# Performance work log

Measured on AMD Instinct MI355X. Metric: run time of the kernel, lower is better.

Reference implementation:

```python
import jax, jax.numpy as jnp
import numpy as np

B, S, D = 4, 2048, 512
H = 8
HD = D // H  # 64
F = 2048
EPS = 1e-12


def _layer_norm(x, g, b):
    mu = jnp.mean(x, axis=-1, keepdims=True)
    var = jnp.mean((x - mu) ** 2, axis=-1, keepdims=True)
    return (x - mu) * jax.lax.rsqrt(var + EPS) * g + b


def setup_inputs() -> dict:
    key = jax.random.key(0)
    ks = jax.random.split(key, 16)
    sd = 0.02
    inp = {
        "x": jax.random.normal(ks[0], (B, S, D), dtype=jnp.float32),
        # per-head q/k/v projections stacked: [H, D, HD] weights, [H, HD] biases
        "Wq": jax.random.normal(ks[1], (H, D, HD), dtype=jnp.float32) * sd,
        "bq": jnp.zeros((H, HD), dtype=jnp.float32),
        "Wk": jax.random.normal(ks[2], (H, D, HD), dtype=jnp.float32) * sd,
        "bk": jnp.zeros((H, HD), dtype=jnp.float32),
        "Wv": jax.random.normal(ks[3], (H, D, HD), dtype=jnp.float32) * sd,
        "bv": jnp.zeros((H, HD), dtype=jnp.float32),
        "Wo": jax.random.normal(ks[4], (D, D), dtype=jnp.float32) * sd,
        "bo": jnp.zeros((D,), dtype=jnp.float32),
        "W1": jax.random.normal(ks[5], (D, F), dtype=jnp.float32) * sd,
        "b1": jnp.zeros((F,), dtype=jnp.float32),
        "W2": jax.random.normal(ks[6], (F, D), dtype=jnp.float32) * sd,
        "b2": jnp.zeros((D,), dtype=jnp.float32),
        "ln1_g": jnp.ones((D,), dtype=jnp.float32),
        "ln1_b": jnp.zeros((D,), dtype=jnp.float32),
        "ln2_g": jnp.ones((D,), dtype=jnp.float32),
        "ln2_b": jnp.zeros((D,), dtype=jnp.float32),
    }
    return inp


def reference(x, Wq, bq, Wk, bk, Wv, bv, Wo, bo, W1, b1, W2, b2,
              ln1_g, ln1_b, ln2_g, ln2_b):
    # Multi-head attention: per-head Linear projections, batched over heads.
    q = jnp.einsum('bsd,hde->bhse', x, Wq) + bq[None, :, None, :]
    k = jnp.einsum('bsd,hde->bhse', x, Wk) + bk[None, :, None, :]
    v = jnp.einsum('bsd,hde->bhse', x, Wv) + bv[None, :, None, :]
    scores = jnp.einsum('bhse,bhte->bhst', q, k) / jnp.sqrt(jnp.float32(HD))
    weights = jax.nn.softmax(scores, axis=-1)  # [B,H,S,S] -- dominant traffic
    attn = jnp.einsum('bhst,bhte->bhse', weights, v)
    # concat heads in order along feature dim -> [B,S,D]
    concat = jnp.transpose(attn, (0, 2, 1, 3)).reshape(B, S, D)
    attn_out = concat @ Wo + bo
    # post-LN residual 1
    x1 = _layer_norm(x + attn_out, ln1_g, ln1_b)
    # FFN (exact GELU, matching torch nn.GELU default)
    h = jax.nn.gelu(x1 @ W1 + b1, approximate=False)
    ff = h @ W2 + b2
    # post-LN residual 2
    return _layer_norm(x1 + ff, ln2_g, ln2_b)
```

## Files before the change

### kernel.cpp

```cpp
#include <hip/hip_runtime.h>
#include <math.h>

#define Bb 4
#define Ss 2048
#define Dd 512
#define Hh 8
#define HDd 64
#define Ff 2048

typedef __bf16 bf16x8 __attribute__((ext_vector_type(8)));
typedef float  f32x4  __attribute__((ext_vector_type(4)));

__device__ __forceinline__ float gelu_f(float x) {
    return 0.5f * x * (1.0f + erff(x * 0.70710678118654752440f));
}

__device__ __forceinline__ unsigned short bfbits(float f) {
    __bf16 h = (__bf16)f;
    return __builtin_bit_cast(unsigned short, h);
}

__device__ __forceinline__ float b2f(unsigned short u) {
    return (float)__builtin_bit_cast(__bf16, u);
}

__device__ __forceinline__ void gld16(const unsigned short* g, unsigned short* l) {
    __builtin_amdgcn_global_load_lds(
        (const __attribute__((address_space(1))) unsigned int*)g,
        (__attribute__((address_space(3))) unsigned int*)l, 16, 0, 0);
}

__device__ __forceinline__ void tile_tconv(
    const float* __restrict__ in, unsigned short* __restrict__ out,
    int R, int C, int c0, int r0)
{
    __shared__ float tile[32][33];
    const int tx = threadIdx.x & 31, ty = threadIdx.x >> 5;
    #pragma unroll
    for (int rr = ty; rr < 32; rr += 8)
        tile[rr][tx] = in[(size_t)(r0 + rr) * C + c0 + tx];
    __syncthreads();
    #pragma unroll
    for (int cc = ty; cc < 32; cc += 8)
        out[(size_t)(c0 + cc) * R + r0 + tx] = bfbits(tile[tx][cc]);
}

__global__ __launch_bounds__(256) void prep_kernel(
    const float* __restrict__ Wq, const float* __restrict__ Wk,
    const float* __restrict__ Wv, const float* __restrict__ Wo,
    const float* __restrict__ W1, const float* __restrict__ W2,
    const float* __restrict__ x,
    unsigned short* __restrict__ WqT, unsigned short* __restrict__ WkT,
    unsigned short* __restrict__ WvT, unsigned short* __restrict__ WoT,
    unsigned short* __restrict__ W1T, unsigned short* __restrict__ W2T,
    unsigned short* __restrict__ xb)
{
    const int bid = blockIdx.x;
    if (bid < 768) {
        const float* src = bid < 256 ? Wq : (bid < 512 ? Wk : Wv);
        unsigned short* dst = bid < 256 ? WqT : (bid < 512 ? WkT : WvT);
        const int local = bid & 255;
        const int z = local >> 5;
        const int rem = local & 31;
        tile_tconv(src + (size_t)z * Dd * HDd, dst + (size_t)z * Dd * HDd,
                   Dd, HDd, (rem & 1) * 32, (rem >> 1) * 32);
    } else if (bid < 1024) {
        const int local = bid - 768;
        tile_tconv(Wo, WoT, Dd, Dd, (local & 15) * 32, (local >> 4) * 32);
    } else if (bid < 2048) {
        const int local = bid - 1024;
        tile_tconv(W1, W1T, Dd, Ff, (local & 63) * 32, (local >> 6) * 32);
    } else if (bid < 3072) {
        const int local = bid - 2048;
        tile_tconv(W2, W2T, Ff, Dd, (local & 15) * 32, (local >> 4) * 32);
    } else {
        const size_t i = ((size_t)(bid - 3072) * 256 + threadIdx.x) * 8;
        float4 a = *(const float4*)(x + i);
        float4 b = *(const float4*)(x + i + 4);
        union { unsigned short us[8]; uint4 u; } p;
        p.us[0] = bfbits(a.x); p.us[1] = bfbits(a.y);
        p.us[2] = bfbits(a.z); p.us[3] = bfbits(a.w);
        p.us[4] = bfbits(b.x); p.us[5] = bfbits(b.y);
        p.us[6] = bfbits(b.z); p.us[7] = bfbits(b.w);
        *(uint4*)(xb + i) = p.u;
    }
}

template<int ACT, int OUTBF>
__global__ __launch_bounds__(256) void gemm_mfma(
    const unsigned short* __restrict__ A, const unsigned short* __restrict__ Bt,
    const float* __restrict__ bias, void* __restrict__ C,
    int M, int N, int K)
{
    __shared__ unsigned short Asb[128 * 32];
    __shared__ unsigned short Bsb[128 * 32];
    const int t    = threadIdx.x;
    const int lane = t & 63;
    const int w    = t >> 6;
    const int ln15 = lane & 15;
    const int quad = lane >> 4;
    const int mw = (w & 1) * 64;
    const int nw = (w >> 1) * 64;
    const int m0 = blockIdx.y * 128;
    const int n0 = blockIdx.x * 128;

    const int r0c = t >> 2,           ch0 = (t & 3) << 3;
    const int r1c = (t + 256) >> 2,   ch1 = ch0;

    f32x4 acc[4][4];
    #pragma unroll
    for (int i = 0; i < 4; i++)
        #pragma unroll
        for (int j = 0; j < 4; j++) acc[i][j] = (f32x4){0.f, 0.f, 0.f, 0.f};

    for (int k0 = 0; k0 < K; k0 += 32) {
        gld16(A  + (size_t)(m0 + r0c) * K + k0 + ch0, &Asb[t * 8]);
        gld16(A  + (size_t)(m0 + r1c) * K + k0 + ch1, &Asb[(t + 256) * 8]);
        gld16(Bt + (size_t)(n0 + r0c) * K + k0 + ch0, &Bsb[t * 8]);
        gld16(Bt + (size_t)(n0 + r1c) * K + k0 + ch1, &Bsb[(t + 256) * 8]);
        __syncthreads();
        bf16x8 af[4], bf[4];
        const int kcol = quad * 8;
        #pragma unroll
        for (int i = 0; i < 4; i++)
            af[i] = *(const bf16x8*)&Asb[(mw + i * 16 + ln15) * 32 + kcol];
        #pragma unroll
        for (int j = 0; j < 4; j++)
            bf[j] = *(const bf16x8*)&Bsb[(nw + j * 16 + ln15) * 32 + kcol];
        #pragma unroll
        for (int i = 0; i < 4; i++)
            #pragma unroll
            for (int j = 0; j < 4; j++)
                acc[i][j] = __builtin_amdgcn_mfma_f32_16x16x32_bf16(
                    af[i], bf[j], acc[i][j], 0, 0, 0);
        __syncthreads();
    }

    #pragma unroll
    for (int i = 0; i < 4; i++) {
        #pragma unroll
        for (int r = 0; r < 4; r++) {
            const int m = m0 + mw + i * 16 + quad * 4 + r;
            #pragma unroll
            for (int j = 0; j < 4; j++) {
                const int n = n0 + nw + j * 16 + ln15;
                float val = acc[i][j][r] + bias[n];
                if (ACT) val = gelu_f(val);
                if (OUTBF)
                    ((unsigned short*)C)[(size_t)m * N + n] = bfbits(val);
                else
                    ((float*)C)[(size_t)m * N + n] = val;
            }
        }
    }
}

__global__ __launch_bounds__(256) void gemm_sk(
    const unsigned short* __restrict__ A, const unsigned short* __restrict__ Bt,
    const float* __restrict__ bias,
    unsigned short* __restrict__ C0, unsigned short* __restrict__ C1,
    int M, int N, int leadK, int Kslice)
{
    __shared__ unsigned short Asb[128 * 32];
    __shared__ unsigned short Bsb[128 * 32];
    const int t    = threadIdx.x;
    const int lane = t & 63;
    const int w    = t >> 6;
    const int ln15 = lane & 15;
    const int quad = lane >> 4;
    const int mw = (w & 1) * 64;
    const int nw = (w >> 1) * 64;
    const int m0 = blockIdx.y * 128;
    const int n0 = blockIdx.x * 128;
    const int z  = blockIdx.z;
    const int kbeg = z * Kslice;
    unsigned short* C = z ? C1 : C0;

    const int r0c = t >> 2,           ch0 = (t & 3) << 3;
    const int r1c = (t + 256) >> 2,   ch1 = ch0;

    f32x4 acc[4][4];
    #pragma unroll
    for (int i = 0; i < 4; i++)
        #pragma unroll
        for (int j = 0; j < 4; j++) acc[i][j] = (f32x4){0.f, 0.f, 0.f, 0.f};

    for (int k0 = kbeg; k0 < kbeg + Kslice; k0 += 32) {
        gld16(A  + (size_t)(m0 + r0c) * leadK + k0 + ch0, &Asb[t * 8]);
        gld16(A  + (size_t)(m0 + r1c) * leadK + k0 + ch1, &Asb[(t + 256) * 8]);
        gld16(Bt + (size_t)(n0 + r0c) * leadK + k0 + ch0, &Bsb[t * 8]);
        gld16(Bt + (size_t)(n0 + r1c) * leadK + k0 + ch1, &Bsb[(t + 256) * 8]);
        __syncthreads();
        bf16x8 af[4], bf[4];
        const int kcol = quad * 8;
        #pragma unroll
        for (int i = 0; i < 4; i++)
            af[i] = *(const bf16x8*)&Asb[(mw + i * 16 + ln15) * 32 + kcol];
        #pragma unroll
        for (int j = 0; j < 4; j++)
            bf[j] = *(const bf16x8*)&Bsb[(nw + j * 16 + ln15) * 32 + kcol];
        #pragma unroll
        for (int i = 0; i < 4; i++)
            #pragma unroll
            for (int j = 0; j < 4; j++)
                acc[i][j] = __builtin_amdgcn_mfma_f32_16x16x32_bf16(
                    af[i], bf[j], acc[i][j], 0, 0, 0);
        __syncthreads();
    }

    #pragma unroll
    for (int i = 0; i < 4; i++) {
        #pragma unroll
        for (int r = 0; r < 4; r++) {
            const int m = m0 + mw + i * 16 + quad * 4 + r;
            #pragma unroll
            for (int j = 0; j < 4; j++) {
                const int n = n0 + nw + j * 16 + ln15;
                const float val = acc[i][j][r] + (z == 0 ? bias[n] : 0.f);
                C[(size_t)m * N + n] = bfbits(val);
            }
        }
    }
}

__global__ __launch_bounds__(256) void qkv_mfma(
    const unsigned short* __restrict__ A,
    const unsigned short* __restrict__ WqT, const unsigned short* __restrict__ WkT,
    const unsigned short* __restrict__ WvT,
    const float* __restrict__ bq, const float* __restrict__ bk,
    const float* __restrict__ bv, unsigned short* __restrict__ qkv)
{
    const unsigned short* Bt = blockIdx.z == 0 ? WqT : (blockIdx.z == 1 ? WkT : WvT);
    const float* bias = blockIdx.z == 0 ? bq : (blockIdx.z == 1 ? bk : bv);
    unsigned short* O = qkv + (size_t)blockIdx.z * ((size_t)Bb * Hh * Ss * HDd);
    const float scl = blockIdx.z == 0 ? 0.125f * 1.44269504088896341f : 1.0f;

    __shared__ unsigned short Asb[128 * 32];
    __shared__ unsigned short Bsb[128 * 32];
    const int t    = threadIdx.x;
    const int lane = t & 63;
    const int w    = t >> 6;
    const int ln15 = lane & 15;
    const int quad = lane >> 4;
    const int mw = (w & 1) * 64;
    const int nw = (w >> 1) * 64;
    const int m0 = blockIdx.y * 128;
    const int n0 = blockIdx.x * 128;

    const int r0c = t >> 2,         ch0 = (t & 3) << 3;
    const int r1c = (t + 256) >> 2, ch1 = ch0;

    f32x4 acc[4][4];
    #pragma unroll
    for (int i = 0; i < 4; i++)
        #pragma unroll
        for (int j = 0; j < 4; j++) acc[i][j] = (f32x4){0.f, 0.f, 0.f, 0.f};

    for (int k0 = 0; k0 < Dd; k0 += 32) {
        gld16(A  + (size_t)(m0 + r0c) * Dd + k0 + ch0, &Asb[t * 8]);
        gld16(A  + (size_t)(m0 + r1c) * Dd + k0 + ch1, &Asb[(t + 256) * 8]);
        gld16(Bt + (size_t)(n0 + r0c) * Dd + k0 + ch0, &Bsb[t * 8]);
        gld16(Bt + (size_t)(n0 + r1c) * Dd + k0 + ch1, &Bsb[(t + 256) * 8]);
        __syncthreads();
        bf16x8 af[4], bf[4];
        const int kcol = quad * 8;
        #pragma unroll
        for (int i = 0; i < 4; i++)
            af[i] = *(const bf16x8*)&Asb[(mw + i * 16 + ln15) * 32 + kcol];
        #pragma unroll
        for (int j = 0; j < 4; j++)
            bf[j] = *(const bf16x8*)&Bsb[(nw + j * 16 + ln15) * 32 + kcol];
        #pragma unroll
        for (int i = 0; i < 4; i++)
            #pragma unroll
            for (int j = 0; j < 4; j++)
                acc[i][j] = __builtin_amdgcn_mfma_f32_16x16x32_bf16(
                    af[i], bf[j], acc[i][j], 0, 0, 0);
        __syncthreads();
    }

    if (blockIdx.z == 2) {
        #pragma unroll
        for (int i = 0; i < 4; i++) {
            const int mb = m0 + mw + i * 16 + quad * 4;
            const int bI = mb >> 11;
            const int sI = mb & 2047;
            #pragma unroll
            for (int j = 0; j < 4; j++) {
                const int n = n0 + nw + j * 16 + ln15;
                union { unsigned short us[4]; uint2 u2; } pk;
                #pragma unroll
                for (int r = 0; r < 4; r++)
                    pk.us[r] = bfbits(acc[i][j][r] + bias[n]);
                *(uint2*)&O[(((size_t)bI * Hh + (n >> 6)) * HDd + (n & 63)) * Ss + sI]
                    = pk.u2;
            }
        }
    } else {
        #pragma unroll
        for (int i = 0; i < 4; i++) {
            #pragma unroll
            for (int r = 0; r < 4; r++) {
                const int m  = m0 + mw + i * 16 + quad * 4 + r;
                const int bI = m >> 11;
                const int sI = m & 2047;
                #pragma unroll
                for (int j = 0; j < 4; j++) {
                    const int n = n0 + nw + j * 16 + ln15;
                    const float val = (acc[i][j][r] + bias[n]) * scl;
                    O[(((size_t)bI * Hh + (n >> 6)) * Ss + sI) * HDd + (n & 63)] =
                        bfbits(val);
                }
            }
        }
    }
}

__global__ __launch_bounds__(256) void attn_mfma(
    const unsigned short* __restrict__ q, const unsigned short* __restrict__ k,
    const unsigned short* __restrict__ vt, unsigned short* __restrict__ out)
{
    __shared__ unsigned short Ks[64 * 64];
    __shared__ unsigned short VTs[64 * 64];
    __shared__ unsigned short Ps[64][72];
    __shared__ float lrow[4][16];
    const int t    = threadIdx.x;
    const int lane = t & 63;
    const int w    = t >> 6;
    const int ln15 = lane & 15;
    const int quad = lane >> 4;
    const int qw   = w * 16;
    const int h = blockIdx.y, b = blockIdx.z;
    const int q0 = blockIdx.x * 64;
    const unsigned short* qb  = q  + (((size_t)b * Hh + h) * Ss + q0) * HDd;
    const unsigned short* kb  = k  + ((size_t)b * Hh + h) * Ss * HDd;
    const unsigned short* vtb = vt + ((size_t)b * Hh + h) * HDd * Ss;

    const int sr0 = t >> 3,         sch0 = (t & 7) << 3;
    const int sr1 = (t + 256) >> 3, sch1 = sch0;

    const bf16x8 qf0 = *(const bf16x8*)(qb + (size_t)(qw + ln15) * HDd + quad * 8);
    const bf16x8 qf1 = *(const bf16x8*)(qb + (size_t)(qw + ln15) * HDd + 32 + quad * 8);

    f32x4 o_acc[4];
    #pragma unroll
    for (int s = 0; s < 4; s++) o_acc[s] = (f32x4){0.f, 0.f, 0.f, 0.f};
    float l_run = 0.f;

    for (int kt = 0; kt < Ss; kt += 64) {
        __syncthreads();
        gld16(kb  + (size_t)(kt + sr0) * HDd + sch0, &Ks[t * 8]);
        gld16(kb  + (size_t)(kt + sr1) * HDd + sch1, &Ks[(t + 256) * 8]);
        gld16(vtb + (size_t)sr0 * Ss + kt + sch0, &VTs[t * 8]);
        gld16(vtb + (size_t)sr1 * Ss + kt + sch1, &VTs[(t + 256) * 8]);
        __syncthreads();

        f32x4 sc[4];
        #pragma unroll
        for (int s = 0; s < 4; s++) {
            const bf16x8 ka  = *(const bf16x8*)&Ks[(s * 16 + ln15) * 64 + quad * 8];
            const bf16x8 kb2 = *(const bf16x8*)&Ks[(s * 16 + ln15) * 64 + 32 + quad * 8];
            f32x4 z = (f32x4){0.f, 0.f, 0.f, 0.f};
            z = __builtin_amdgcn_mfma_f32_16x16x32_bf16(ka, qf0, z, 0, 0, 0);
            sc[s] = __builtin_amdgcn_mfma_f32_16x16x32_bf16(kb2, qf1, z, 0, 0, 0);
        }

        #pragma unroll
        for (int s = 0; s < 4; s++)
            #pragma unroll
            for (int r = 0; r < 4; r++) {
                sc[s][r] = exp2f(sc[s][r]);
                l_run += sc[s][r];
            }

        #pragma unroll
        for (int s = 0; s < 4; s++) {
            union { unsigned short us[4]; uint2 u2; } pk;
            #pragma unroll
            for (int r = 0; r < 4; r++) pk.us[r] = bfbits(sc[s][r]);
            *(uint2*)&Ps[qw + ln15][s * 16 + quad * 4] = pk.u2;
        }

        const bf16x8 pf0 = *(const bf16x8*)&Ps[qw + ln15][quad * 8];
        const bf16x8 pf1 = *(const bf16x8*)&Ps[qw + ln15][32 + quad * 8];
        #pragma unroll
        for (int s = 0; s < 4; s++) {
            const bf16x8 v0 = *(const bf16x8*)&VTs[(s * 16 + ln15) * 64 + quad * 8];
            const bf16x8 v1 = *(const bf16x8*)&VTs[(s * 16 + ln15) * 64 + 32 + quad * 8];
            o_acc[s] = __builtin_amdgcn_mfma_f32_16x16x32_bf16(pf0, v0, o_acc[s], 0, 0, 0);
            o_acc[s] = __builtin_amdgcn_mfma_f32_16x16x32_bf16(pf1, v1, o_acc[s], 0, 0, 0);
        }
    }

    l_run += __shfl_xor(l_run, 16);
    l_run += __shfl_xor(l_run, 32);
    if (quad == 0) lrow[w][ln15] = l_run;
    const float4 lv = *(const float4*)&lrow[w][quad * 4];
    const float inv[4] = {1.f / lv.x, 1.f / lv.y, 1.f / lv.z, 1.f / lv.w};
    #pragma unroll
    for (int r = 0; r < 4; r++) {
        const int row = q0 + qw + quad * 4 + r;
        #pragma unroll
        for (int s = 0; s < 4; s++) {
            const int dim = s * 16 + ln15;
            out[((size_t)b * Ss + row) * Dd + h * HDd + dim] =
                bfbits(o_acc[s][r] * inv[r]);
        }
    }
}

template<int WRITE_BF>
__global__ __launch_bounds__(256) void ln_kernel(
    const unsigned short* __restrict__ a0, const unsigned short* __restrict__ a1,
    const float* __restrict__ res,
    const float* __restrict__ g, const float* __restrict__ bb,
    float* __restrict__ out, unsigned short* __restrict__ outb)
{
    const int row = blockIdx.x;
    const int t = threadIdx.x;
    const size_t o0 = (size_t)row * Dd + t;
    const size_t o1 = o0 + 256;
    float v0 = b2f(a0[o0]) + b2f(a1[o0]) + res[o0];
    float v1 = b2f(a0[o1]) + b2f(a1[o1]) + res[o1];

    float sum = v0 + v1;
    #pragma unroll
    for (int o = 32; o; o >>= 1) sum += __shfl_down(sum, o);
    __shared__ float red1[4], red2[4];
    const int wid = t >> 6, lane = t & 63;
    if (!lane) red1[wid] = sum;
    __syncthreads();
    sum = red1[0] + red1[1] + red1[2] + red1[3];
    const float mu = sum * (1.0f / Dd);

    const float d0 = v0 - mu, d1 = v1 - mu;
    float sq = d0 * d0 + d1 * d1;
    #pragma unroll
    for (int o = 32; o; o >>= 1) sq += __shfl_down(sq, o);
    if (!lane) red2[wid] = sq;
    __syncthreads();
    sq = red2[0] + red2[1] + red2[2] + red2[3];
    const float rstd = rsqrtf(sq * (1.0f / Dd) + 1e-12f);

    const float y0 = d0 * rstd * g[t] + bb[t];
    const float y1 = d1 * rstd * g[t + 256] + bb[t + 256];
    out[o0] = y0;
    out[o1] = y1;
    if (WRITE_BF) {
        outb[o0] = bfbits(y0);
        outb[o1] = bfbits(y1);
    }
}

extern "C" void kernel_launch(void* const* d_in, const int* in_sizes, int n_in,
                              void* d_out, int out_size, void* d_ws, size_t ws_size,
                              hipStream_t stream) {
    const float* x   = (const float*)d_in[0];
    const float* Wq  = (const float*)d_in[1];
    const float* bq  = (const float*)d_in[2];
    const float* Wk  = (const float*)d_in[3];
    const float* bk  = (const float*)d_in[4];
    const float* Wv  = (const float*)d_in[5];
    const float* bv  = (const float*)d_in[6];
    const float* Wo  = (const float*)d_in[7];
    const float* bo  = (const float*)d_in[8];
    const float* W1  = (const float*)d_in[9];
    const float* b1  = (const float*)d_in[10];
    const float* W2  = (const float*)d_in[11];
    const float* b2  = (const float*)d_in[12];
    const float* g1  = (const float*)d_in[13];
    const float* be1 = (const float*)d_in[14];
    const float* g2  = (const float*)d_in[15];
    const float* be2 = (const float*)d_in[16];
    float* out = (float*)d_out;

    const size_t NT = (size_t)Bb * Ss * Dd;
    unsigned short* wsu = (unsigned short*)d_ws;
    unsigned short* qkvb  = wsu;
    unsigned short* projA = wsu + 3 * NT;
    unsigned short* projB = wsu + 4 * NT;
    unsigned short* hb    = wsu + 3 * NT;
    unsigned short* actb  = wsu + 7 * NT;
    unsigned short* x1b   = wsu + 8 * NT;
    unsigned short* ff0   = wsu;
    unsigned short* ff1   = wsu + NT;
    float* x1 = (float*)(wsu + 9 * NT);
    unsigned short* wpool = wsu + 11 * NT;
    unsigned short* WqT = wpool;
    unsigned short* WkT = wpool + 262144;
    unsigned short* WvT = wpool + 524288;
    unsigned short* WoT = wpool + 786432;
    unsigned short* W1T = wpool + 1048576;
    unsigned short* W2T = wpool + 2097152;
    const int M = Bb * Ss;

    prep_kernel<<<5120, 256, 0, stream>>>(
        Wq, Wk, Wv, Wo, W1, W2, x,
        WqT, WkT, WvT, WoT, W1T, W2T, actb);

    qkv_mfma<<<dim3(Dd / 128, M / 128, 3), 256, 0, stream>>>(
        actb, WqT, WkT, WvT, bq, bk, bv, qkvb);

    attn_mfma<<<dim3(Ss / 64, Hh, Bb), 256, 0, stream>>>(
        qkvb, qkvb + NT, qkvb + 2 * NT, actb);

    gemm_sk<<<dim3(Dd / 128, M / 128, 2), 256, 0, stream>>>(
        actb, WoT, bo, projA, projB, M, Dd, Dd, Dd / 2);

    ln_kernel<1><<<M, 256, 0, stream>>>(projA, projB, x, g1, be1, x1, x1b);

    gemm_mfma<1, 1><<<dim3(Ff / 128, M / 128), 256, 0, stream>>>(
        x1b, W1T, b1, hb, M, Ff, Dd);

    gemm_sk<<<dim3(Dd / 128, M / 128, 2), 256, 0, stream>>>(
        hb, W2T, b2, ff0, ff1, M, Dd, Ff, Ff / 2);

    ln_kernel<0><<<M, 256, 0, stream>>>(ff0, ff1, x1, g2, be2, out, nullptr);
}
```

Baseline: 336.2 us.

## Split attention over two key halves with separate combine kernel and padded LDS

Splits each attention block's key range into two halves, launched as separate blocks, so the grid doubles. Each half writes an unnormalized bf16 partial output and its row sums, and a new combine kernel adds the halves and normalizes. K/V tiles move from async global-to-LDS loads to register-staged copies into padded [64][72] LDS arrays, which should reduce bank conflicts. The cost is an extra kernel launch, extra partial-output traffic, and a second bf16 rounding of the partial outputs.

```diff
diff --git a/kernel.cpp b/kernel.cpp
--- a/kernel.cpp
+++ b/kernel.cpp
@@ -318,27 +318,26 @@
 
 __global__ __launch_bounds__(256) void attn_mfma(
     const unsigned short* __restrict__ q, const unsigned short* __restrict__ k,
-    const unsigned short* __restrict__ vt, unsigned short* __restrict__ out)
-{
-    __shared__ unsigned short Ks[64 * 64];
-    __shared__ unsigned short VTs[64 * 64];
+    const unsigned short* __restrict__ vt,
+    unsigned short* __restrict__ opart, float* __restrict__ lpart)
+{
+    __shared__ unsigned short Ks[64][72];
+    __shared__ unsigned short VTs[64][72];
     __shared__ unsigned short Ps[64][72];
-    __shared__ float lrow[4][16];
     const int t    = threadIdx.x;
     const int lane = t & 63;
     const int w    = t >> 6;
     const int ln15 = lane & 15;
     const int quad = lane >> 4;
     const int qw   = w * 16;
-    const int h = blockIdx.y, b = blockIdx.z;
+    const int h    = blockIdx.y;
+    const int b    = blockIdx.z >> 1;
+    const int half = blockIdx.z & 1;
     const int q0 = blockIdx.x * 64;
     const unsigned short* qb  = q  + (((size_t)b * Hh + h) * Ss + q0) * HDd;
     const unsigned short* kb  = k  + ((size_t)b * Hh + h) * Ss * HDd;
     const unsigned short* vtb = vt + ((size_t)b * Hh + h) * HDd * Ss;
 
-    const int sr0 = t >> 3,         sch0 = (t & 7) << 3;
-    const int sr1 = (t + 256) >> 3, sch1 = sch0;
-
     const bf16x8 qf0 = *(const bf16x8*)(qb + (size_t)(qw + ln15) * HDd + quad * 8);
     const bf16x8 qf1 = *(const bf16x8*)(qb + (size_t)(qw + ln15) * HDd + 32 + quad * 8);
 
@@ -347,19 +346,25 @@
     for (int s = 0; s < 4; s++) o_acc[s] = (f32x4){0.f, 0.f, 0.f, 0.f};
     float l_run = 0.f;
 
-    for (int kt = 0; kt < Ss; kt += 64) {
-        __syncthreads();
-        gld16(kb  + (size_t)(kt + sr0) * HDd + sch0, &Ks[t * 8]);
-        gld16(kb  + (size_t)(kt + sr1) * HDd + sch1, &Ks[(t + 256) * 8]);
-        gld16(vtb + (size_t)sr0 * Ss + kt + sch0, &VTs[t * 8]);
-        gld16(vtb + (size_t)sr1 * Ss + kt + sch1, &VTs[(t + 256) * 8]);
+    const int kbeg = half * (Ss / 2);
+    for (int kt = kbeg; kt < kbeg + Ss / 2; kt += 64) {
+        __syncthreads();
+        #pragma unroll
+        for (int p = 0; p < 2; p++) {
+            const int u = p * 256 + t;
+            const int row = u >> 3, ch = u & 7;
+            *(bf16x8*)&Ks[row][ch * 8] =
+                *(const bf16x8*)(kb + (size_t)(kt + row) * HDd + ch * 8);
+            *(bf16x8*)&VTs[row][ch * 8] =
+                *(const bf16x8*)(vtb + (size_t)row * Ss + kt + ch * 8);
+        }
         __syncthreads();
 
         f32x4 sc[4];
         #pragma unroll
         for (int s = 0; s < 4; s++) {
-            const bf16x8 ka  = *(const bf16x8*)&Ks[(s * 16 + ln15) * 64 + quad * 8];
-            const bf16x8 kb2 = *(const bf16x8*)&Ks[(s * 16 + ln15) * 64 + 32 + quad * 8];
+            const bf16x8 ka  = *(const bf16x8*)&Ks[s * 16 + ln15][quad * 8];
+            const bf16x8 kb2 = *(const bf16x8*)&Ks[s * 16 + ln15][32 + quad * 8];
             f32x4 z = (f32x4){0.f, 0.f, 0.f, 0.f};
             z = __builtin_amdgcn_mfma_f32_16x16x32_bf16(ka, qf0, z, 0, 0, 0);
             sc[s] = __builtin_amdgcn_mfma_f32_16x16x32_bf16(kb2, qf1, z, 0, 0, 0);
@@ -385,8 +390,8 @@
         const bf16x8 pf1 = *(const bf16x8*)&Ps[qw + ln15][32 + quad * 8];
         #pragma unroll
         for (int s = 0; s < 4; s++) {
-            const bf16x8 v0 = *(const bf16x8*)&VTs[(s * 16 + ln15) * 64 + quad * 8];
-            const bf16x8 v1 = *(const bf16x8*)&VTs[(s * 16 + ln15) * 64 + 32 + quad * 8];
+            const bf16x8 v0 = *(const bf16x8*)&VTs[s * 16 + ln15][quad * 8];
+            const bf16x8 v1 = *(const bf16x8*)&VTs[s * 16 + ln15][32 + quad * 8];
             o_acc[s] = __builtin_amdgcn_mfma_f32_16x16x32_bf16(pf0, v0, o_acc[s], 0, 0, 0);
             o_acc[s] = __builtin_amdgcn_mfma_f32_16x16x32_bf16(pf1, v1, o_acc[s], 0, 0, 0);
         }
@@ -394,19 +399,42 @@
 
     l_run += __shfl_xor(l_run, 16);
     l_run += __shfl_xor(l_run, 32);
-    if (quad == 0) lrow[w][ln15] = l_run;
-    const float4 lv = *(const float4*)&lrow[w][quad * 4];
-    const float inv[4] = {1.f / lv.x, 1.f / lv.y, 1.f / lv.z, 1.f / lv.w};
+    if (quad == 0)
+        lpart[(((size_t)half * Bb + b) * Hh + h) * Ss + q0 + qw + ln15] = l_run;
+
+    unsigned short* ob = opart + (size_t)half * ((size_t)Bb * Ss * Dd);
     #pragma unroll
     for (int r = 0; r < 4; r++) {
         const int row = q0 + qw + quad * 4 + r;
         #pragma unroll
         for (int s = 0; s < 4; s++) {
             const int dim = s * 16 + ln15;
-            out[((size_t)b * Ss + row) * Dd + h * HDd + dim] =
-                bfbits(o_acc[s][r] * inv[r]);
-        }
-    }
+            ob[((size_t)b * Ss + row) * Dd + h * HDd + dim] = bfbits(o_acc[s][r]);
+        }
+    }
+}
+
+__global__ __launch_bounds__(256) void attn_combine(
+    const unsigned short* __restrict__ op, const float* __restrict__ lpart,
+    unsigned short* __restrict__ out)
+{
+    const int t   = threadIdx.x;
+    const int row = blockIdx.x * 4 + (t >> 6);
+    const int b   = row >> 11, s = row & 2047;
+    const int e0  = (t & 63) * 8;
+    const int h   = e0 >> 6;
+    const size_t NTc = (size_t)Bb * Ss * Dd;
+    const float l = lpart[((size_t)b * Hh + h) * Ss + s]
+                  + lpart[(((size_t)Bb + b) * Hh + h) * Ss + s];
+    const float inv = 1.f / l;
+    const size_t base = (size_t)row * Dd + e0;
+    union { unsigned short us[8]; uint4 u; } ua, uc, uo;
+    ua.u = *(const uint4*)(op + base);
+    uc.u = *(const uint4*)(op + NTc + base);
+    #pragma unroll
+    for (int i = 0; i < 8; i++)
+        uo.us[i] = bfbits((b2f(ua.us[i]) + b2f(uc.us[i])) * inv);
+    *(uint4*)(out + base) = uo.u;
 }
 
 template<int WRITE_BF>
@@ -477,6 +505,7 @@
     const size_t NT = (size_t)Bb * Ss * Dd;
     unsigned short* wsu = (unsigned short*)d_ws;
     unsigned short* qkvb  = wsu;
+    unsigned short* opart = wsu + 3 * NT;
     unsigned short* projA = wsu + 3 * NT;
     unsigned short* projB = wsu + 4 * NT;
     unsigned short* hb    = wsu + 3 * NT;
@@ -492,6 +521,7 @@
     unsigned short* WoT = wpool + 786432;
     unsigned short* W1T = wpool + 1048576;
     unsigned short* W2T = wpool + 2097152;
+    float* lpart = (float*)(wpool + 3145728);
     const int M = Bb * Ss;
 
     prep_kernel<<<5120, 256, 0, stream>>>(
@@ -501,8 +531,9 @@
     qkv_mfma<<<dim3(Dd / 128, M / 128, 3), 256, 0, stream>>>(
         actb, WqT, WkT, WvT, bq, bk, bv, qkvb);
 
-    attn_mfma<<<dim3(Ss / 64, Hh, Bb), 256, 0, stream>>>(
-        qkvb, qkvb + NT, qkvb + 2 * NT, actb);
+    attn_mfma<<<dim3(Ss / 64, Hh, Bb * 2), 256, 0, stream>>>(
+        qkvb, qkvb + NT, qkvb + 2 * NT, opart, lpart);
+    attn_combine<<<M / 4, 256, 0, stream>>>(opart, lpart, actb);
 
     gemm_sk<<<dim3(Dd / 128, M / 128, 2), 256, 0, stream>>>(
         actb, WoT, bo, projA, projB, M, Dd, Dd, Dd / 2);
```

Measured after the change: 332.3 us. About the same (-1.2%).
